# Performance work log

Measured on AMD Instinct MI355X. Metric: run time of the kernel, lower is better.

The kernel has to match this reference:

```python
import jax, jax.numpy as jnp
import numpy as np

B, N, D_MODEL, H = 8, 1024, 768, 12
HD = D_MODEL // H  # head dim = 64
SCALE = D_MODEL ** (-0.5)  # NOTE: original scales by input_dim**-0.5, not head_dim**-0.5


def setup_inputs() -> dict:
    key = jax.random.key(0)
    k1, k2 = jax.random.split(key)
    x = jax.random.normal(k1, (B, N, D_MODEL), dtype=jnp.float32)
    # torch Linear weight is [out,in]; we store transposed [in,out] for x @ W
    w_qkv = jax.random.normal(k2, (D_MODEL, 3 * D_MODEL), dtype=jnp.float32) * (D_MODEL ** -0.5)
    b_qkv = jnp.zeros((3 * D_MODEL,), dtype=jnp.float32)
    return {"x": x, "w_qkv": w_qkv, "b_qkv": b_qkv}


def reference(x, w_qkv, b_qkv):
    # QKV projection: [B, N, 3*D]
    y = jnp.einsum("bnd,de->bne", x, w_qkv) + b_qkv
    # Faithful to einops 'b n (h d qkv) -> qkv b h n d': qkv is fastest-varying
    y = y.reshape(B, N, H, HD, 3)
    q = jnp.transpose(y[..., 0], (0, 2, 1, 3))  # [B, H, N, HD]
    k = jnp.transpose(y[..., 1], (0, 2, 1, 3))
    v = jnp.transpose(y[..., 2], (0, 2, 1, 3))
    energy = jnp.einsum("bhqd,bhkd->bhqk", q, k)
    attn = jax.nn.softmax(energy * SCALE, axis=-1)  # dropout is identity at eval
    out = jnp.einsum("bhqk,bhkd->bhqd", attn, v)
    # 'b h n d -> b n (h d)'
    return jnp.transpose(out, (0, 2, 1, 3)).reshape(B, N, D_MODEL)
```

## Files before the change

kernel.cpp:

```cpp
#include <hip/hip_runtime.h>
#include <hip/hip_bf16.h>
#include <stdint.h>

#define NB 8
#define NS 1024
#define DM 768
#define NH 12
#define DH 64
#define NE 2304
#define MTOT (NB*NS)

typedef unsigned short u16;
typedef __attribute__((ext_vector_type(8))) __bf16 bf16x8;
typedef __attribute__((ext_vector_type(4))) float floatx4;
typedef __attribute__((ext_vector_type(4))) uint32_t uint32x4;

#define WS_XB  0ull
#define WS_WT  12582912ull
#define WS_QB  16121856ull
#define WS_KB  28704768ull
#define WS_VT  41287680ull

#define QSC 0.05206490030275093f

__device__ __forceinline__ u16 f2bf(float f) {
  union { float f; uint32_t u; } v; v.f = f;
  uint32_t r = (v.u + 0x7fffu + ((v.u >> 16) & 1u)) >> 16;
  return (u16)r;
}

__device__ __forceinline__ void gload16(const void* g, void* l) {
  __builtin_amdgcn_global_load_lds(
      (const __attribute__((address_space(1))) void*)g,
      (__attribute__((address_space(3))) void*)l, 16, 0, 0);
}

__global__ void conv_x_kernel(const float4* __restrict__ x, u16* __restrict__ xb, int n4) {
  int i = blockIdx.x * blockDim.x + threadIdx.x;
  int stride = gridDim.x * blockDim.x;
  for (; i < n4; i += stride) {
    float4 v = x[i];
    ushort4 r;
    r.x = f2bf(v.x); r.y = f2bf(v.y); r.z = f2bf(v.z); r.w = f2bf(v.w);
    ((ushort4*)xb)[i] = r;
  }
}

__global__ void transpose_w_kernel(const float* __restrict__ w, u16* __restrict__ wt) {
  __shared__ float tile[32][33];
  const int e0 = blockIdx.x * 32, k0 = blockIdx.y * 32;
  const int tx = threadIdx.x, ty = threadIdx.y;
#pragma unroll
  for (int i = 0; i < 4; i++)
    tile[ty + i*8][tx] = w[(size_t)(k0 + ty + i*8) * NE + e0 + tx];
  __syncthreads();
#pragma unroll
  for (int i = 0; i < 4; i++)
    wt[(size_t)(e0 + ty + i*8) * DM + k0 + tx] = f2bf(tile[tx][ty + i*8]);
}

__global__ __launch_bounds__(256) void qkv_gemm_kernel(
    const u16* __restrict__ xb, const u16* __restrict__ wt,
    const float* __restrict__ bias,
    u16* __restrict__ qb, u16* __restrict__ kb, u16* __restrict__ vtb) {
  __shared__ __align__(16) u16 a_lds[128 * 32];
  __shared__ __align__(16) u16 b_lds[128 * 32];
  const int t  = threadIdx.x;
  const int w  = t >> 6, l = t & 63;
  const int wr = w >> 1, wc = w & 1;
  const int lq = l & 15, lg = l >> 4;
  const int m0 = (int)(blockIdx.x % 64) * 128;
  const int n0 = (int)(blockIdx.x / 64) * 128;

  floatx4 z = {0.f, 0.f, 0.f, 0.f};
  floatx4 acc[4][4];
#pragma unroll
  for (int i = 0; i < 4; i++)
#pragma unroll
    for (int j = 0; j < 4; j++) acc[i][j] = z;

  const int srow = t >> 2;
  const int scb  = (t & 3) ^ ((t >> 3) & 3);
  const u16* ga = xb + (size_t)m0 * DM + scb * 8;
  const u16* gb = wt + (size_t)n0 * DM + scb * 8;
  const int rswz = (lq >> 1) & 3;

  for (int k0 = 0; k0 < DM; k0 += 32) {
#pragma unroll
    for (int i = 0; i < 2; i++) {
      gload16(ga + (size_t)(i*64 + srow) * DM + k0, (char*)a_lds + i*4096 + w*1024);
      gload16(gb + (size_t)(i*64 + srow) * DM + k0, (char*)b_lds + i*4096 + w*1024);
    }
    __syncthreads();

    bf16x8 af[4], bfr[4];
#pragma unroll
    for (int i = 0; i < 4; i++)
      af[i] = *(const bf16x8*)((const char*)a_lds + (wr*64 + i*16 + lq)*64 + ((lg ^ rswz) * 16));
#pragma unroll
    for (int j = 0; j < 4; j++)
      bfr[j] = *(const bf16x8*)((const char*)b_lds + (wc*64 + j*16 + lq)*64 + ((lg ^ rswz) * 16));
#pragma unroll
    for (int i = 0; i < 4; i++)
#pragma unroll
      for (int j = 0; j < 4; j++)
        acc[i][j] = __builtin_amdgcn_mfma_f32_16x16x32_bf16(af[i], bfr[j], acc[i][j], 0, 0, 0);
    __syncthreads();
  }

#pragma unroll
  for (int j = 0; j < 4; j++) {
    const int gn = n0 + wc*64 + j*16 + lq;
    const float bv = bias[gn];
    const int qkv = gn % 3;
    const int h   = gn / 192;
    const int d   = (gn % 192) / 3;
#pragma unroll
    for (int i = 0; i < 4; i++) {
      const int gmb = m0 + wr*64 + i*16 + lg*4;
#pragma unroll
      for (int r = 0; r < 4; r++) {
        const int gm = gmb + r;
        const int bb = gm >> 10, nn = gm & 1023;
        const int bh = bb * NH + h;
        float ov = acc[i][j][r] + bv;
        if (qkv == 0) ov *= QSC;
        const u16 val = f2bf(ov);
        if (qkv == 0)      qb[((size_t)bh * NS + nn) * DH + d] = val;
        else if (qkv == 1) kb[((size_t)bh * NS + nn) * DH + d] = val;
        else               vtb[((size_t)bh * DH + d) * NS + nn] = val;
      }
    }
  }
}

__global__ __launch_bounds__(256) void attn_kernel(
    const u16* __restrict__ qb, const u16* __restrict__ kb,
    const u16* __restrict__ vtb, float* __restrict__ out) {
  __shared__ __align__(16) u16 k_lds[64 * 64];
  __shared__ __align__(16) u16 v_lds[64 * 64];

  const int t = threadIdx.x, w = t >> 6, l = t & 63;
  const int bh = blockIdx.x >> 3, qblk = blockIdx.x & 7;
  const int bb = bh / NH, h = bh % NH;
  const int q0 = qblk * 128 + w * 32;
  const int lq = l & 15, lg = l >> 4;

  bf16x8 qf[2][2];
#pragma unroll
  for (int qt = 0; qt < 2; qt++) {
    const u16* qrow = qb + ((size_t)bh * NS + q0 + qt*16 + lq) * DH;
#pragma unroll
    for (int ds = 0; ds < 2; ds++)
      qf[qt][ds] = *(const bf16x8*)&qrow[lg*8 + ds*32];
  }

  float m2[2]    = {4.0f, 4.0f};
  float lsumP[2] = {0.f, 0.f};
  floatx4 z = {0.f, 0.f, 0.f, 0.f};
  floatx4 o[2][4];
#pragma unroll
  for (int qt = 0; qt < 2; qt++)
#pragma unroll
    for (int dt = 0; dt < 4; dt++) o[qt][dt] = z;

  const int srow = t >> 3;
  const int scb  = (t & 7) ^ (srow & 7);

  for (int kt0 = 0; kt0 < 16; kt0++) {
    const int k0 = kt0 * 64;
    __syncthreads();
#pragma unroll
    for (int i = 0; i < 2; i++) {
      const int row = i*32 + srow;
      gload16(kb  + ((size_t)bh * NS + k0 + row) * DH + scb*8, (char*)k_lds + i*4096 + w*1024);
      gload16(vtb + ((size_t)bh * DH + row) * NS + k0 + scb*8, (char*)v_lds + i*4096 + w*1024);
    }
    __syncthreads();

#pragma unroll
    for (int half = 0; half < 2; half++) {
      bf16x8 kf[2][2];
#pragma unroll
      for (int kt = 0; kt < 2; kt++) {
        const int krow = half*32 + ((lq >> 2) << 3) + kt*4 + (lq & 3);
#pragma unroll
        for (int ds = 0; ds < 2; ds++)
          kf[kt][ds] = *(const bf16x8*)((const char*)k_lds + krow*128 + ((ds*4 + lg) ^ (krow & 7))*16);
      }
      bf16x8 vf[4];
#pragma unroll
      for (int dt = 0; dt < 4; dt++) {
        const int vrow = dt*16 + lq;
        vf[dt] = *(const bf16x8*)((const char*)v_lds + vrow*128 + ((half*4 + lg) ^ (vrow & 7))*16);
      }

#pragma unroll
      for (int qt = 0; qt < 2; qt++) {
        floatx4 st0 = z, st1 = z;
        st0 = __builtin_amdgcn_mfma_f32_16x16x32_bf16(kf[0][0], qf[qt][0], st0, 0, 0, 0);
        st0 = __builtin_amdgcn_mfma_f32_16x16x32_bf16(kf[0][1], qf[qt][1], st0, 0, 0, 0);
        st1 = __builtin_amdgcn_mfma_f32_16x16x32_bf16(kf[1][0], qf[qt][0], st1, 0, 0, 0);
        st1 = __builtin_amdgcn_mfma_f32_16x16x32_bf16(kf[1][1], qf[qt][1], st1, 0, 0, 0);

        float p[8];
#pragma unroll
        for (int r = 0; r < 4; r++) { p[r] = st0[r]; p[4 + r] = st1[r]; }
        const float pmax = fmaxf(fmaxf(fmaxf(p[0], p[1]), fmaxf(p[2], p[3])),
                                 fmaxf(fmaxf(p[4], p[5]), fmaxf(p[6], p[7])));

        if (!__all(pmax - m2[qt] <= 8.0f)) {
          float mt = pmax;
          mt = fmaxf(mt, __shfl_xor(mt, 16));
          mt = fmaxf(mt, __shfl_xor(mt, 32));
          const float mnew = fmaxf(m2[qt], mt);
          const float corr = exp2f(m2[qt] - mnew);
          lsumP[qt] *= corr;
          float cr[4];
#pragma unroll
          for (int r = 0; r < 4; r++) cr[r] = __shfl(corr, lg*4 + r);
#pragma unroll
          for (int dt = 0; dt < 4; dt++)
#pragma unroll
            for (int r = 0; r < 4; r++) o[qt][dt][r] *= cr[r];
          m2[qt] = mnew;
        }

        const float m = m2[qt];
        float ls = 0.f;
        u16 pb[8];
#pragma unroll
        for (int e = 0; e < 8; e++) {
          const float pe = exp2f(p[e] - m);
          ls += pe;
          pb[e] = f2bf(pe);
        }
        lsumP[qt] += ls;

        uint32x4 pw;
        pw.x = (uint32_t)pb[0] | ((uint32_t)pb[1] << 16);
        pw.y = (uint32_t)pb[2] | ((uint32_t)pb[3] << 16);
        pw.z = (uint32_t)pb[4] | ((uint32_t)pb[5] << 16);
        pw.w = (uint32_t)pb[6] | ((uint32_t)pb[7] << 16);
        const bf16x8 pa = __builtin_bit_cast(bf16x8, pw);

#pragma unroll
        for (int dt = 0; dt < 4; dt++)
          o[qt][dt] = __builtin_amdgcn_mfma_f32_16x16x32_bf16(pa, vf[dt], o[qt][dt], 0, 0, 0);
      }
    }
  }

#pragma unroll
  for (int qt = 0; qt < 2; qt++) {
    float ls = lsumP[qt];
    ls += __shfl_xor(ls, 16);
    ls += __shfl_xor(ls, 32);
    const float inv = 1.0f / ls;
    float ir[4];
#pragma unroll
    for (int r = 0; r < 4; r++) ir[r] = __shfl(inv, lg*4 + r);
#pragma unroll
    for (int dt = 0; dt < 4; dt++)
#pragma unroll
      for (int r = 0; r < 4; r++) {
        const int n = q0 + qt*16 + lg*4 + r;
        out[((size_t)bb * NS + n) * DM + h*DH + dt*16 + lq] = o[qt][dt][r] * ir[r];
      }
  }
}

extern "C" void kernel_launch(void* const* d_in, const int* in_sizes, int n_in,
                              void* d_out, int out_size, void* d_ws, size_t ws_size,
                              hipStream_t stream) {
  const float* x     = (const float*)d_in[0];
  const float* w_qkv = (const float*)d_in[1];
  const float* b_qkv = (const float*)d_in[2];
  float* out = (float*)d_out;
  char* ws = (char*)d_ws;

  u16* xb  = (u16*)(ws + WS_XB);
  u16* wt  = (u16*)(ws + WS_WT);
  u16* qb  = (u16*)(ws + WS_QB);
  u16* kb  = (u16*)(ws + WS_KB);
  u16* vtb = (u16*)(ws + WS_VT);

  conv_x_kernel<<<1024, 256, 0, stream>>>((const float4*)x, xb, MTOT * DM / 4);
  transpose_w_kernel<<<dim3(NE/32, DM/32), dim3(32, 8), 0, stream>>>(w_qkv, wt);
  qkv_gemm_kernel<<<64 * (NE/128), 256, 0, stream>>>(xb, wt, b_qkv, qb, kb, vtb);
  attn_kernel<<<(NB*NH) * (NS/128), 256, 0, stream>>>(qb, kb, vtb, out);
}
```

Baseline: 122.5 us.

## Permute QKV weight columns so GEMM epilogue writes contiguous Q/K/V tiles

Reorders the transposed weight so each 128-column GEMM tile belongs to a single Q, K or V class with contiguous head dims, and folds the Q scale into the weights and a preprocessed bias. The V class swaps the MFMA operands so the transposed V store is contiguous along the sequence. This is meant to replace scattered per-element stores with class-dependent branching by coalesced writes. It adds a small bias-prep kernel and changes the grid to 3D, which also changes block scheduling order.

```diff
diff --git a/kernel.cpp b/kernel.cpp
--- a/kernel.cpp
+++ b/kernel.cpp
@@ -17,9 +17,10 @@
 
 #define WS_XB  0ull
 #define WS_WT  12582912ull
-#define WS_QB  16121856ull
-#define WS_KB  28704768ull
-#define WS_VT  41287680ull
+#define WS_BR  16121856ull
+#define WS_QB  16131072ull
+#define WS_KB  28713984ull
+#define WS_VT  41296896ull
 
 #define QSC 0.05206490030275093f
 
@@ -46,22 +47,37 @@
   }
 }
 
+__global__ void prep_bias_kernel(const float* __restrict__ b, float* __restrict__ br) {
+  const int o = blockIdx.x * 256 + threadIdx.x;
+  if (o < 3 * DM) {
+    const int c = o / DM, n = o % DM;
+    const int h = n >> 6, d = n & 63;
+    float v = b[h * 192 + d * 3 + c];
+    if (c == 0) v *= QSC;
+    br[o] = v;
+  }
+}
+
 __global__ void transpose_w_kernel(const float* __restrict__ w, u16* __restrict__ wt) {
   __shared__ float tile[32][33];
-  const int e0 = blockIdx.x * 32, k0 = blockIdx.y * 32;
+  const int c  = blockIdx.z;
+  const int n0 = blockIdx.x * 32, k0 = blockIdx.y * 32;
   const int tx = threadIdx.x, ty = threadIdx.y;
+  const int n_in = n0 + tx;
+  const int ecol = (n_in >> 6) * 192 + (n_in & 63) * 3 + c;
+  const float sc = (c == 0) ? QSC : 1.0f;
 #pragma unroll
   for (int i = 0; i < 4; i++)
-    tile[ty + i*8][tx] = w[(size_t)(k0 + ty + i*8) * NE + e0 + tx];
+    tile[ty + i*8][tx] = w[(size_t)(k0 + ty + i*8) * NE + ecol];
   __syncthreads();
 #pragma unroll
   for (int i = 0; i < 4; i++)
-    wt[(size_t)(e0 + ty + i*8) * DM + k0 + tx] = f2bf(tile[tx][ty + i*8]);
+    wt[((size_t)c * DM + n0 + ty + i*8) * DM + k0 + tx] = f2bf(tile[tx][ty + i*8] * sc);
 }
 
 __global__ __launch_bounds__(256) void qkv_gemm_kernel(
     const u16* __restrict__ xb, const u16* __restrict__ wt,
-    const float* __restrict__ bias,
+    const float* __restrict__ br,
     u16* __restrict__ qb, u16* __restrict__ kb, u16* __restrict__ vtb) {
   __shared__ __align__(16) u16 a_lds[128 * 32];
   __shared__ __align__(16) u16 b_lds[128 * 32];
@@ -69,8 +85,9 @@
   const int w  = t >> 6, l = t & 63;
   const int wr = w >> 1, wc = w & 1;
   const int lq = l & 15, lg = l >> 4;
-  const int m0 = (int)(blockIdx.x % 64) * 128;
-  const int n0 = (int)(blockIdx.x / 64) * 128;
+  const int m0  = (int)blockIdx.x * 128;
+  const int n0  = (int)blockIdx.y * 128;
+  const int cls = (int)blockIdx.z;
 
   floatx4 z = {0.f, 0.f, 0.f, 0.f};
   floatx4 acc[4][4];
@@ -82,7 +99,7 @@
   const int srow = t >> 2;
   const int scb  = (t & 3) ^ ((t >> 3) & 3);
   const u16* ga = xb + (size_t)m0 * DM + scb * 8;
-  const u16* gb = wt + (size_t)n0 * DM + scb * 8;
+  const u16* gb = wt + ((size_t)cls * DM + n0) * DM + scb * 8;
   const int rswz = (lq >> 1) & 3;
 
   for (int k0 = 0; k0 < DM; k0 += 32) {
@@ -100,35 +117,57 @@
 #pragma unroll
     for (int j = 0; j < 4; j++)
       bfr[j] = *(const bf16x8*)((const char*)b_lds + (wc*64 + j*16 + lq)*64 + ((lg ^ rswz) * 16));
-#pragma unroll
-    for (int i = 0; i < 4; i++)
-#pragma unroll
-      for (int j = 0; j < 4; j++)
-        acc[i][j] = __builtin_amdgcn_mfma_f32_16x16x32_bf16(af[i], bfr[j], acc[i][j], 0, 0, 0);
+    if (cls == 2) {
+#pragma unroll
+      for (int i = 0; i < 4; i++)
+#pragma unroll
+        for (int j = 0; j < 4; j++)
+          acc[i][j] = __builtin_amdgcn_mfma_f32_16x16x32_bf16(bfr[j], af[i], acc[i][j], 0, 0, 0);
+    } else {
+#pragma unroll
+      for (int i = 0; i < 4; i++)
+#pragma unroll
+        for (int j = 0; j < 4; j++)
+          acc[i][j] = __builtin_amdgcn_mfma_f32_16x16x32_bf16(af[i], bfr[j], acc[i][j], 0, 0, 0);
+    }
     __syncthreads();
   }
 
-#pragma unroll
-  for (int j = 0; j < 4; j++) {
-    const int gn = n0 + wc*64 + j*16 + lq;
-    const float bv = bias[gn];
-    const int qkv = gn % 3;
-    const int h   = gn / 192;
-    const int d   = (gn % 192) / 3;
-#pragma unroll
-    for (int i = 0; i < 4; i++) {
-      const int gmb = m0 + wr*64 + i*16 + lg*4;
-#pragma unroll
-      for (int r = 0; r < 4; r++) {
-        const int gm = gmb + r;
-        const int bb = gm >> 10, nn = gm & 1023;
-        const int bh = bb * NH + h;
-        float ov = acc[i][j][r] + bv;
-        if (qkv == 0) ov *= QSC;
-        const u16 val = f2bf(ov);
-        if (qkv == 0)      qb[((size_t)bh * NS + nn) * DH + d] = val;
-        else if (qkv == 1) kb[((size_t)bh * NS + nn) * DH + d] = val;
-        else               vtb[((size_t)bh * DH + d) * NS + nn] = val;
+  if (cls != 2) {
+    u16* dst = (cls == 0) ? qb : kb;
+#pragma unroll
+    for (int j = 0; j < 4; j++) {
+      const int n  = n0 + wc*64 + j*16 + lq;
+      const int h  = n >> 6, d = n & 63;
+      const float bv = br[cls * DM + n];
+#pragma unroll
+      for (int i = 0; i < 4; i++) {
+        const int mb = m0 + wr*64 + i*16 + lg*4;
+#pragma unroll
+        for (int r = 0; r < 4; r++) {
+          const int m = mb + r;
+          const int bb = m >> 10, nn = m & 1023;
+          dst[(((size_t)(bb * NH + h)) * NS + nn) * DH + d] = f2bf(acc[i][j][r] + bv);
+        }
+      }
+    }
+  } else {
+    const int hq = (n0 + wc*64) >> 6;
+#pragma unroll
+    for (int j = 0; j < 4; j++) {
+      float bvv[4];
+#pragma unroll
+      for (int r = 0; r < 4; r++)
+        bvv[r] = br[2 * DM + n0 + wc*64 + j*16 + lg*4 + r];
+#pragma unroll
+      for (int i = 0; i < 4; i++) {
+        const int m = m0 + wr*64 + i*16 + lq;
+        const int bb = m >> 10, nn = m & 1023;
+#pragma unroll
+        for (int r = 0; r < 4; r++) {
+          const int d = (wc*64 + j*16 + lg*4 + r) & 63;
+          vtb[(((size_t)(bb * NH + hq)) * DH + d) * NS + nn] = f2bf(acc[i][j][r] + bvv[r]);
+        }
       }
     }
   }
@@ -279,14 +318,16 @@
   float* out = (float*)d_out;
   char* ws = (char*)d_ws;
 
-  u16* xb  = (u16*)(ws + WS_XB);
-  u16* wt  = (u16*)(ws + WS_WT);
-  u16* qb  = (u16*)(ws + WS_QB);
-  u16* kb  = (u16*)(ws + WS_KB);
-  u16* vtb = (u16*)(ws + WS_VT);
+  u16* xb   = (u16*)(ws + WS_XB);
+  u16* wt   = (u16*)(ws + WS_WT);
+  float* br = (float*)(ws + WS_BR);
+  u16* qb   = (u16*)(ws + WS_QB);
+  u16* kb   = (u16*)(ws + WS_KB);
+  u16* vtb  = (u16*)(ws + WS_VT);
 
   conv_x_kernel<<<1024, 256, 0, stream>>>((const float4*)x, xb, MTOT * DM / 4);
-  transpose_w_kernel<<<dim3(NE/32, DM/32), dim3(32, 8), 0, stream>>>(w_qkv, wt);
-  qkv_gemm_kernel<<<64 * (NE/128), 256, 0, stream>>>(xb, wt, b_qkv, qb, kb, vtb);
+  prep_bias_kernel<<<9, 256, 0, stream>>>(b_qkv, br);
+  transpose_w_kernel<<<dim3(DM/32, DM/32, 3), dim3(32, 8), 0, stream>>>(w_qkv, wt);
+  qkv_gemm_kernel<<<dim3(MTOT/128, DM/128, 3), 256, 0, stream>>>(xb, wt, br, qb, kb, vtb);
   attn_kernel<<<(NB*NH) * (NS/128), 256, 0, stream>>>(qb, kb, vtb, out);
 }
```

Measured after the change: 149.9 us. 1.22x slower.
